# Kernel tuning notes

Hardware: AMD Instinct MI355X
Metric: run time of the kernel (lower is better)

The kernel has to match this reference:

```python
import jax, jax.numpy as jnp
import numpy as np

NF, NG, NH, NR, HS = 6, 32, 16, 15, 256
NT, NS = 1000, 2000


def _linear_init(k, fan_in, fan_out):
    s = 1.0 / np.sqrt(fan_in)
    kw, kb = jax.random.split(k)
    W = jax.random.uniform(kw, (fan_in, fan_out), minval=-s, maxval=s, dtype=jnp.float32)
    b = jax.random.uniform(kb, (fan_out,), minval=-s, maxval=s, dtype=jnp.float32)
    return W, b


def setup_inputs() -> dict:
    key = jax.random.key(0)
    ks = jax.random.split(key, 12)
    # forcings: Prcp, Evp, T1(min temp), T2(max temp), Rad, Hum; ensure Prcp>=0 and T2>T1
    base = jax.random.normal(ks[0], (NT, NS)) * 10.0
    spread = jax.random.uniform(ks[1], (NT, NS)) * 5.0 + 0.5
    prcp = jax.random.uniform(ks[2], (NT, NS)) * 10.0
    evp = jax.random.uniform(ks[3], (NT, NS)) * 3.0
    rad = jax.random.uniform(ks[4], (NT, NS))
    hum = jax.random.uniform(ks[5], (NT, NS))
    x = jnp.stack([prcp, evp, base - spread, base + spread, rad, hum], axis=-1).astype(jnp.float32)
    xc = jax.random.normal(ks[6], (NS, NG), dtype=jnp.float32)
    W_fc, b_fc = _linear_init(ks[7], NG, HS)
    W_r, b_r = _linear_init(ks[8], HS, NH * (NR + 1))
    W_g, b_g = _linear_init(ks[9], HS, NH * 9)
    W_kin, b_kin = _linear_init(ks[10], 4, HS)
    W_kout, b_kout = _linear_init(ks[11], HS, NH * 1)
    return dict(x=x, xc=xc, W_fc=W_fc, b_fc=b_fc, W_r=W_r, b_r=b_r,
                W_g=W_g, b_g=b_g, W_kin=W_kin, b_kin=b_kin,
                W_kout=W_kout, b_kout=b_kout)


def reference(x, xc, W_fc, b_fc, W_r, b_r, W_g, b_g, W_kin, b_kin, W_kout, b_kout):
    nt, ns, _ = x.shape
    Prcp, Evp, T1, T2 = x[..., 0], x[..., 1], x[..., 2], x[..., 3]
    f = x[..., 2:]                                   # [nt, ns, 4]

    # --- getParam (eval mode: DropMask is identity) ---
    state = xc @ W_fc + b_fc                         # [ns, hs]
    pK = jnp.tanh(f @ W_kin + b_kin + state) @ W_kout + b_kout   # [nt, ns, nh]
    km = jnp.exp(pK)                                 # melt rate per step
    g = jnp.tanh(state)
    pG = g @ W_g + b_g                               # [ns, 9*nh]
    sl = lambda i: pG[..., i * NH:(i + 1) * NH]
    kp = jax.nn.sigmoid(sl(0))
    ks_ = jax.nn.sigmoid(sl(1))
    kd = jax.nn.sigmoid(sl(2))
    gd = jax.nn.sigmoid(sl(3))
    gl = (jax.nn.sigmoid(sl(4)) * 10.0) ** 3
    qb = jax.nn.relu(sl(5)) / 10.0
    ga = jax.nn.softmax(sl(6), axis=-1)
    gi = jnp.clip(sl(7) / 6.0 + 0.5, 0.0, 1.0) / 2.0   # hardsigmoid/2
    ge = jax.nn.relu(sl(8))

    # one-peak routing weights over nr lags: [nr, ns, nh], sums to 1 over lag
    pR = (g @ W_r + b_r).reshape(ns, NH, NR + 1)
    loc = jax.nn.sigmoid(pR[..., 0]) * NR            # peak location in [0, nr]
    lags = jnp.arange(NR, dtype=x.dtype)
    wR = jax.nn.softmax(pR[..., 1:] - (lags - loc[..., None]) ** 2, axis=-1)
    paramR = jnp.transpose(wR, (2, 0, 1))            # [nr, ns, nh]

    # --- divideP: split precip into snow / liquid by the fraction of [T1,T2] above 0C ---
    vL = jnp.clip(T2 / jnp.maximum(T2 - T1, 1e-6), 0.0, 1.0)
    Pl = (Prcp * vL)[..., None]                      # [nt, ns, 1]
    Ps = (Prcp * (1.0 - vL))[..., None]
    Ev = Evp[..., None]

    # --- bucket.step recurrence over time via scan ---
    def step(carry, inp):
        Sf, Ss, Sd = carry
        ps, pl, ev, kmt = inp
        Sf1 = Sf + ps                                # snow bucket
        qf = jnp.minimum(Sf1, kmt)                   # melt
        Sf2 = Sf1 - qf
        Pin = pl + qf                                # liquid input
        H = jax.nn.relu(Ss + Pin * (1.0 - gi) - ev * ge)   # shallow bucket
        qp = jax.nn.relu(H - gl) * kp                # saturation-excess quick flow
        qo = jnp.minimum(H, gl) * ks_                # shallow drainage
        Ss2 = H - qp - qo
        D = Sd + Pin * gi + qo * gd                  # deep bucket
        qd = D * kd + qb                             # baseflow
        Sd2 = D * (1.0 - kd)
        qTot = qp + qo * (1.0 - gd) + qd             # qp + qs + qd
        return (Sf2, Ss2, Sd2), qTot

    z = jnp.zeros((ns, NH), dtype=x.dtype)
    _, qTot = jax.lax.scan(step, (z, z, z), (Ps, Pl, Ev, km))   # [nt, ns, nh]

    # --- windowed routing convolution + mixture over buckets ---
    # out[j, s] = sum_{i<nr} sum_h qTot[j+i, s, h] * paramR[i, s, h] * ga[s, h]
    W = paramR * ga[None]                            # [nr, ns, nh]
    L = nt - NR + 1
    out = jnp.zeros((L, ns), dtype=x.dtype)
    for i in range(NR):                              # small fixed lag loop
        out = out + jnp.einsum('tsh,sh->ts', qTot[i:i + L], W[i])
    return out
```

## Files before the change

kernel.cpp:

```cpp
#include <hip/hip_runtime.h>
#include <hip/hip_bf16.h>
#include <hip/hip_fp16.h>

#define NG 32
#define NH 16
#define NR 15
#define HS 256
#define NT 1000
#define NS 2000
#define LOUT (NT - NR + 1)
#define TC 40
#define SPB 8
#define NCH (NT / TC)
#define NTP 1001

typedef __attribute__((ext_vector_type(8))) short bhalf8;
typedef __attribute__((ext_vector_type(4))) float f32x4;
typedef __attribute__((ext_vector_type(2))) float f32x2;
typedef __attribute__((ext_vector_type(4))) unsigned short us4;
typedef __attribute__((ext_vector_type(8))) unsigned short us8;

__device__ __forceinline__ float fast_rcp(float x) { return __builtin_amdgcn_rcpf(x); }
__device__ __forceinline__ float fast_tanh(float x) {
    float e = __expf(2.0f * x);
    return 1.0f - 2.0f * fast_rcp(e + 1.0f);
}
__device__ __forceinline__ float fast_sigmoid(float x) {
    return fast_rcp(1.0f + __expf(-x));
}
__device__ __forceinline__ short f2bf(float f) {
    __bf16 h = (__bf16)f;
    return __builtin_bit_cast(short, h);
}
__device__ __forceinline__ float h2f(unsigned short u) {
    return (float)__builtin_bit_cast(_Float16, u);
}
__device__ __forceinline__ unsigned short f2h(float f) {
    return __builtin_bit_cast(unsigned short, (_Float16)f);
}

__global__ __launch_bounds__(256) void k_prep(const float* __restrict__ x,
                                              float* __restrict__ xT) {
    int s0 = blockIdx.x * 16;
    int t0 = blockIdx.y * 64;
    int tid = threadIdx.x;
    __shared__ float sX[64][97];
    for (int g = tid; g < 64 * 24; g += 256) {
        int tl = g / 24, c4 = g - tl * 24;
        if (t0 + tl < NT) {
            float4 v = *(const float4*)(x + ((size_t)(t0 + tl) * NS + s0) * 6 + c4 * 4);
            sX[tl][c4 * 4 + 0] = v.x;
            sX[tl][c4 * 4 + 1] = v.y;
            sX[tl][c4 * 4 + 2] = v.z;
            sX[tl][c4 * 4 + 3] = v.w;
        }
    }
    __syncthreads();
    int tl = tid & 63;
    int t = t0 + tl;
    if (t < NT) {
#pragma unroll
        for (int p = 0; p < 4; ++p) {
            int sl = (tid >> 6) + p * 4;
            const float* r = &sX[tl][sl * 6];
            size_t base = ((size_t)(s0 + sl) * 6) * NT + t;
            xT[base + 0 * NT] = r[0];
            xT[base + 1 * NT] = r[1];
            xT[base + 2 * NT] = r[2];
            xT[base + 3 * NT] = r[3];
            xT[base + 4 * NT] = r[4];
            xT[base + 5 * NT] = r[5];
        }
    }
}

__global__ __launch_bounds__(256) void k_site(
    const float* __restrict__ xc, const float* __restrict__ W_fc, const float* __restrict__ b_fc,
    const float* __restrict__ W_r, const float* __restrict__ b_r,
    const float* __restrict__ W_g, const float* __restrict__ b_g,
    const float* __restrict__ b_kin,
    float* __restrict__ state2, float* __restrict__ params, float* __restrict__ wfir)
{
    int s = blockIdx.x, tid = threadIdx.x;
    __shared__ float sXc[NG];
    __shared__ float sG[HS];
    __shared__ float sPG[144];
    __shared__ float sPR[256];
    if (tid < NG) sXc[tid] = xc[s * NG + tid];
    __syncthreads();
    float st = b_fc[tid];
#pragma unroll
    for (int g = 0; g < NG; ++g) st += sXc[g] * W_fc[g * HS + tid];
    state2[s * HS + tid] = st + b_kin[tid];
    float gv = fast_tanh(st);
    sG[tid] = gv;
    __syncthreads();
    {
        float a = b_r[tid];
#pragma unroll 8
        for (int u = 0; u < HS; ++u) a += sG[u] * W_r[u * 256 + tid];
        sPR[tid] = a;
    }
    if (tid < 144) {
        float a = b_g[tid];
#pragma unroll 8
        for (int u = 0; u < HS; ++u) a += sG[u] * W_g[u * 144 + tid];
        sPG[tid] = a;
    }
    __syncthreads();
    if (tid < NH) {
        int h = tid;
        float m = -1e30f;
        for (int k = 0; k < NH; ++k) m = fmaxf(m, sPG[96 + k]);
        float sum = 0.f;
        for (int k = 0; k < NH; ++k) sum += __expf(sPG[96 + k] - m);
        float ga = __expf(sPG[96 + h] - m) * fast_rcp(sum);
        float kp = fast_sigmoid(sPG[h]);
        float ks = fast_sigmoid(sPG[16 + h]);
        float kd = fast_sigmoid(sPG[32 + h]);
        float gd = fast_sigmoid(sPG[48 + h]);
        float glv = fast_sigmoid(sPG[64 + h]) * 10.0f;
        float gl = glv * glv * glv;
        float qb = fmaxf(sPG[80 + h], 0.f) * 0.1f;
        float gi = fminf(fmaxf(sPG[112 + h] * (1.0f / 6.0f) + 0.5f, 0.f), 1.f) * 0.5f;
        float ge = fmaxf(sPG[128 + h], 0.f);
        float* P = params + s * 128;
        P[0 * 16 + h] = kp;  P[1 * 16 + h] = ks;  P[2 * 16 + h] = kd;  P[3 * 16 + h] = gd;
        P[4 * 16 + h] = gl;  P[5 * 16 + h] = qb;  P[6 * 16 + h] = gi;  P[7 * 16 + h] = ge;
        float loc = fast_sigmoid(sPR[h * 16 + 0]) * 15.0f;
        float l[NR];
        float mm = -1e30f;
#pragma unroll
        for (int i = 0; i < NR; ++i) {
            float d = (float)i - loc;
            l[i] = sPR[h * 16 + 1 + i] - d * d;
            mm = fmaxf(mm, l[i]);
        }
        float ssum = 0.f;
#pragma unroll
        for (int i = 0; i < NR; ++i) { l[i] = __expf(l[i] - mm); ssum += l[i]; }
        float r = fast_rcp(ssum) * ga;
#pragma unroll
        for (int i = 0; i < NR; ++i) wfir[s * (NR * NH) + i * NH + h] = l[i] * r;
    }
}

__global__ __launch_bounds__(256) void k_km(
    const float* __restrict__ xT, const float* __restrict__ state2,
    const float* __restrict__ W_kin, const float* __restrict__ W_kout,
    const float* __restrict__ b_kout, _Float16* __restrict__ kmh)
{
    const float Ck = 2.8853900817779268f;
    int s = blockIdx.x, tid = threadIdx.x;
    int wave = tid >> 6, lane = tid & 63;
    int r15 = lane & 15, kg = lane >> 4;

    f32x2 st[2][4], w0[2][4], w1[2][4], w2[2][4], w3[2][4];
    bhalf8 Bf[2];
    float csp = 0.f;
#pragma unroll
    for (int q = 0; q < 2; ++q) {
        int u0 = (2 * wave + q) * 32 + kg * 8;
#pragma unroll
        for (int e = 0; e < 4; ++e) {
            int u = u0 + 2 * e;
            st[q][e] = *(const f32x2*)(state2 + s * HS + u) * Ck;
            w0[q][e] = *(const f32x2*)(W_kin + 0 * HS + u) * Ck;
            w1[q][e] = *(const f32x2*)(W_kin + 1 * HS + u) * Ck;
            w2[q][e] = *(const f32x2*)(W_kin + 2 * HS + u) * Ck;
            w3[q][e] = *(const f32x2*)(W_kin + 3 * HS + u) * Ck;
            float wa = W_kout[(u)     * NH + r15];
            float wb = W_kout[(u + 1) * NH + r15];
            csp += wa + wb;
            Bf[q][2 * e]     = f2bf(-2.0f * wa);
            Bf[q][2 * e + 1] = f2bf(-2.0f * wb);
        }
    }
    __shared__ float sCS[4][4][16];
    sCS[wave][kg][r15] = csp;
    __syncthreads();
    float bk2 = b_kout[r15];
#pragma unroll
    for (int w = 0; w < 4; ++w)
#pragma unroll
        for (int k = 0; k < 4; ++k) bk2 += sCS[w][k][r15];

    const float* fpl = xT + ((size_t)s * 6 + 2) * NT;
    _Float16* kp = kmh + (size_t)s * NT * NH;

    __shared__ f32x4 sRed[2][4][4][64];

    for (int tg = 0; tg < 16; ++tg) {
        int buf = tg & 1;
#pragma unroll
        for (int tile = 0; tile < 4; ++tile) {
            int t = tg * 64 + tile * 16 + r15;
            int tcl = t < NT ? t : NT - 1;
            float f0 = fpl[tcl];
            float f1 = fpl[NT + tcl];
            float f2 = fpl[2 * NT + tcl];
            float f3 = fpl[3 * NT + tcl];
            f32x4 acc = {0.f, 0.f, 0.f, 0.f};
#pragma unroll
            for (int q = 0; q < 2; ++q) {
                bhalf8 A;
#pragma unroll
                for (int e = 0; e < 4; ++e) {
                    f32x2 p = st[q][e];
                    p += f0 * w0[q][e];
                    p += f1 * w1[q][e];
                    p += f2 * w2[q][e];
                    p += f3 * w3[q][e];
                    f32x2 ex = {__builtin_amdgcn_exp2f(p.x), __builtin_amdgcn_exp2f(p.y)};
                    f32x2 e1 = ex + 1.0f;
                    A[2 * e]     = f2bf(fast_rcp(e1.x));
                    A[2 * e + 1] = f2bf(fast_rcp(e1.y));
                }
                acc = __builtin_amdgcn_mfma_f32_16x16x32_bf16(A, Bf[q], acc, 0, 0, 0);
            }
            sRed[buf][tile][wave][lane] = acc;
        }
        __syncthreads();
        {
            f32x4 a0 = sRed[buf][wave][0][lane];
            f32x4 a1 = sRed[buf][wave][1][lane];
            f32x4 a2 = sRed[buf][wave][2][lane];
            f32x4 a3 = sRed[buf][wave][3][lane];
            f32x4 acc = (a0 + a1) + (a2 + a3);
            int tb = tg * 64 + wave * 16;
#pragma unroll
            for (int j = 0; j < 4; ++j) {
                int tt = tb + kg * 4 + j;
                if (tt < NT) kp[(size_t)tt * NH + r15] = (_Float16)__expf(acc[j] + bk2);
            }
        }
    }
}

__global__ __launch_bounds__(128) void k_scan(
    const float* __restrict__ params, const float* __restrict__ xT,
    _Float16* __restrict__ kmh)
{
    int tid = threadIdx.x;
    int sl = tid >> 4, h = tid & 15;
    int S0 = blockIdx.x * SPB;
    __shared__ __align__(16) unsigned short sKmH[2][TC][128];
    __shared__ __align__(16) float sF[2][3][SPB][TC];

    const float* P = params + (size_t)(S0 + sl) * 128;
    float kp = P[h], ks = P[16 + h], kd = P[32 + h], gd = P[48 + h];
    float gl = P[64 + h], qb = P[80 + h], gi = P[96 + h], ge = P[112 + h];
    float gi1 = 1.f - gi, gd1 = 1.f - gd, kd1 = 1.f - kd;
    float Sf = 0.f, Ss = 0.f, Sd = 0.f;

    us4 vkm[10];
    float4 fP, fE, fT1, fT2;
    int fsite = tid / 10, ftcq = tid - fsite * 10;
    size_t fbase = ((size_t)(S0 + (fsite < SPB ? fsite : 0)) * 6) * NT + ftcq * 4;

    auto LOAD = [&](int t0) {
#pragma unroll
        for (int r = 0; r < 10; ++r) {
            int g = r * 128 + tid;
            int site = g / 160;
            int rem = g - site * 160;
            int tc = rem >> 2, h0 = (rem & 3) << 2;
            vkm[r] = *(const us4*)(kmh + (((size_t)(S0 + site) * NT + t0 + tc) * NH + h0));
        }
        if (tid < 80) {
            fP  = *(const float4*)(xT + fbase + t0);
            fE  = *(const float4*)(xT + fbase + (size_t)NT + t0);
            fT1 = *(const float4*)(xT + fbase + 2 * (size_t)NT + t0);
            fT2 = *(const float4*)(xT + fbase + 3 * (size_t)NT + t0);
        }
    };
    auto STORE_LDS = [&](int b) {
#pragma unroll
        for (int r = 0; r < 10; ++r) {
            int g = r * 128 + tid;
            int site = g / 160;
            int rem = g - site * 160;
            int tc = rem >> 2, h0 = (rem & 3) << 2;
            *(us4*)&sKmH[b][tc][site * 16 + h0] = vkm[r];
        }
        if (tid < 80) {
            float4 ps, pl;
            {
                float den = fmaxf(fT2.x - fT1.x, 1e-6f);
                float vL = fminf(fmaxf(fT2.x * fast_rcp(den), 0.f), 1.f);
                pl.x = fP.x * vL; ps.x = fP.x - pl.x;
            }
            {
                float den = fmaxf(fT2.y - fT1.y, 1e-6f);
                float vL = fminf(fmaxf(fT2.y * fast_rcp(den), 0.f), 1.f);
                pl.y = fP.y * vL; ps.y = fP.y - pl.y;
            }
            {
                float den = fmaxf(fT2.z - fT1.z, 1e-6f);
                float vL = fminf(fmaxf(fT2.z * fast_rcp(den), 0.f), 1.f);
                pl.z = fP.z * vL; ps.z = fP.z - pl.z;
            }
            {
                float den = fmaxf(fT2.w - fT1.w, 1e-6f);
                float vL = fminf(fmaxf(fT2.w * fast_rcp(den), 0.f), 1.f);
                pl.w = fP.w * vL; ps.w = fP.w - pl.w;
            }
            *(float4*)&sF[b][0][fsite][ftcq * 4] = ps;
            *(float4*)&sF[b][1][fsite][ftcq * 4] = pl;
            *(float4*)&sF[b][2][fsite][ftcq * 4] = fE;
        }
    };

    size_t qbase = ((size_t)(S0 + sl) * NT) * NH + h;

    LOAD(0);
    STORE_LDS(0);
    __syncthreads();
    for (int c = 0; c < NCH; ++c) {
        int b = c & 1;
        if (c + 1 < NCH) LOAD((c + 1) * TC);
        int t0 = c * TC;
#pragma unroll 8
        for (int tc = 0; tc < TC; ++tc) {
            float ps = sF[b][0][sl][tc], pl = sF[b][1][sl][tc], ev = sF[b][2][sl][tc];
            float kmv = h2f(sKmH[b][tc][tid]);
            Sf += ps;
            float qf = fminf(Sf, kmv);
            Sf -= qf;
            float Pin = pl + qf;
            float H = fmaxf(Ss + Pin * gi1 - ev * ge, 0.f);
            float qp = fmaxf(H - gl, 0.f) * kp;
            float qo = fminf(H, gl) * ks;
            Ss = H - qp - qo;
            float D = Sd + Pin * gi + qo * gd;
            float qd = D * kd + qb;
            Sd = D * kd1;
            kmh[qbase + (size_t)(t0 + tc) * NH] = (_Float16)(qp + qo * gd1 + qd);
        }
        if (c + 1 < NCH) {
            STORE_LDS((c + 1) & 1);
            __syncthreads();
        }
    }
}

__global__ __launch_bounds__(256) void k_fir(
    const _Float16* __restrict__ kmh, const float* __restrict__ wfir,
    float* __restrict__ outT)
{
    int s = blockIdx.x, tid = threadIdx.x;
    __shared__ float sQ[NH * NTP];
    __shared__ float sW[NR * NH];
    const us8* src = (const us8*)(kmh + (size_t)s * NT * NH);
    for (int g = tid; g < NT * NH / 8; g += 256) {
        us8 v = src[g];
        int t = g >> 1, h0 = (g & 1) << 3;
#pragma unroll
        for (int e = 0; e < 8; ++e)
            sQ[(h0 + e) * NTP + t] = h2f(v[e]);
    }
    if (tid < NR * NH) sW[tid] = wfir[(size_t)s * NR * NH + tid];
    __syncthreads();
#pragma unroll
    for (int c = 0; c < 4; ++c) {
        int tau = tid + 256 * c;
        if (tau < LOUT) {
            float acc = 0.f;
#pragma unroll
            for (int hh = 0; hh < NH; ++hh) {
                const float* q = sQ + hh * NTP + tau;
#pragma unroll
                for (int i = 0; i < NR; ++i) acc += q[i] * sW[i * 16 + hh];
            }
            outT[(size_t)s * LOUT + tau] = acc;
        }
    }
}

__global__ __launch_bounds__(256) void k_tr(const float* __restrict__ outT,
                                            float* __restrict__ out)
{
    int s0 = blockIdx.x * 64, t0 = blockIdx.y * 16, tid = threadIdx.x;
    __shared__ float sT[16][65];
    for (int g = tid; g < 64 * 16; g += 256) {
        int sl = g >> 4, tl = g & 15;
        int s = s0 + sl, t = t0 + tl;
        sT[tl][sl] = (s < NS && t < LOUT) ? outT[(size_t)s * LOUT + t] : 0.f;
    }
    __syncthreads();
    int ss = tid & 63;
#pragma unroll
    for (int p = 0; p < 4; ++p) {
        int tl = (tid >> 6) + p * 4;
        int t = t0 + tl, s = s0 + ss;
        if (t < LOUT && s < NS) out[(size_t)t * NS + s] = sT[tl][ss];
    }
}

extern "C" void kernel_launch(void* const* d_in, const int* in_sizes, int n_in,
                              void* d_out, int out_size, void* d_ws, size_t ws_size,
                              hipStream_t stream) {
    const float* x      = (const float*)d_in[0];
    const float* xc     = (const float*)d_in[1];
    const float* W_fc   = (const float*)d_in[2];
    const float* b_fc   = (const float*)d_in[3];
    const float* W_r    = (const float*)d_in[4];
    const float* b_r    = (const float*)d_in[5];
    const float* W_g    = (const float*)d_in[6];
    const float* b_g    = (const float*)d_in[7];
    const float* W_kin  = (const float*)d_in[8];
    const float* b_kin  = (const float*)d_in[9];
    const float* W_kout = (const float*)d_in[10];
    const float* b_kout = (const float*)d_in[11];
    float* out = (float*)d_out;

    float* ws     = (float*)d_ws;
    float* state2 = ws;
    float* params = state2 + (size_t)NS * HS;
    float* wfir   = params + (size_t)NS * 128;
    float* xT     = wfir + (size_t)NS * NR * NH;
    _Float16* kmh = (_Float16*)(xT + (size_t)NS * 6 * NT);
    float* outT   = (float*)(kmh + (size_t)NS * NT * NH);

    k_prep<<<dim3(NS / 16, (NT + 63) / 64), 256, 0, stream>>>(x, xT);
    k_site<<<NS, 256, 0, stream>>>(xc, W_fc, b_fc, W_r, b_r, W_g, b_g, b_kin,
                                   state2, params, wfir);
    k_km<<<NS, 256, 0, stream>>>(xT, state2, W_kin, W_kout, b_kout, kmh);
    k_scan<<<NS / SPB, 128, 0, stream>>>(params, xT, kmh);
    k_fir<<<NS, 256, 0, stream>>>(kmh, wfir, outT);
    k_tr<<<dim3((NS + 63) / 64, (LOUT + 15) / 16), 256, 0, stream>>>(outT, out);
}
```

Before: 327.4 us.

## Register-block FIR over four outputs per thread with fp16 LDS storage

The routing FIR kernel now keeps the qTot history in LDS as raw fp16 in padded rows, which halves LDS footprint and allows vectorized 4-wide loads. Each thread computes four consecutive outputs, loading a 20-element window per bucket into registers and reusing it across lags. This cuts the redundant LDS reads of the old one-output-per-thread loop. It costs more registers and adds padding zero-fill and per-element half-to-float conversions in the inner loop.

```diff
diff --git a/kernel.cpp b/kernel.cpp
--- a/kernel.cpp
+++ b/kernel.cpp
@@ -12,7 +12,7 @@
 #define TC 40
 #define SPB 8
 #define NCH (NT / TC)
-#define NTP 1001
+#define QROW 1048
 
 typedef __attribute__((ext_vector_type(8))) short bhalf8;
 typedef __attribute__((ext_vector_type(4))) float f32x4;
@@ -349,32 +349,48 @@
     float* __restrict__ outT)
 {
     int s = blockIdx.x, tid = threadIdx.x;
-    __shared__ float sQ[NH * NTP];
+    __shared__ unsigned short sQ[NH][QROW];
     __shared__ float sW[NR * NH];
+    for (int idx = tid; idx < NH * (QROW - NT); idx += 256) {
+        int h = idx / (QROW - NT), j = idx - h * (QROW - NT);
+        sQ[h][NT + j] = 0;
+    }
     const us8* src = (const us8*)(kmh + (size_t)s * NT * NH);
     for (int g = tid; g < NT * NH / 8; g += 256) {
         us8 v = src[g];
         int t = g >> 1, h0 = (g & 1) << 3;
 #pragma unroll
-        for (int e = 0; e < 8; ++e)
-            sQ[(h0 + e) * NTP + t] = h2f(v[e]);
+        for (int e = 0; e < 8; ++e) sQ[h0 + e][t] = v[e];
     }
     if (tid < NR * NH) sW[tid] = wfir[(size_t)s * NR * NH + tid];
     __syncthreads();
-#pragma unroll
-    for (int c = 0; c < 4; ++c) {
-        int tau = tid + 256 * c;
-        if (tau < LOUT) {
-            float acc = 0.f;
-#pragma unroll
-            for (int hh = 0; hh < NH; ++hh) {
-                const float* q = sQ + hh * NTP + tau;
-#pragma unroll
-                for (int i = 0; i < NR; ++i) acc += q[i] * sW[i * 16 + hh];
-            }
-            outT[(size_t)s * LOUT + tau] = acc;
-        }
-    }
+
+    int tau0 = tid * 4;
+    float a0 = 0.f, a1 = 0.f, a2 = 0.f, a3 = 0.f;
+#pragma unroll
+    for (int h = 0; h < NH; ++h) {
+        float q[20];
+#pragma unroll
+        for (int r = 0; r < 5; ++r) {
+            us4 v = *(const us4*)&sQ[h][tau0 + 4 * r];
+            q[4 * r + 0] = h2f(v[0]);
+            q[4 * r + 1] = h2f(v[1]);
+            q[4 * r + 2] = h2f(v[2]);
+            q[4 * r + 3] = h2f(v[3]);
+        }
+#pragma unroll
+        for (int i = 0; i < NR; ++i) {
+            float w = sW[i * 16 + h];
+            a0 += q[i] * w;
+            a1 += q[i + 1] * w;
+            a2 += q[i + 2] * w;
+            a3 += q[i + 3] * w;
+        }
+    }
+    if (tau0 + 0 < LOUT) outT[(size_t)s * LOUT + tau0 + 0] = a0;
+    if (tau0 + 1 < LOUT) outT[(size_t)s * LOUT + tau0 + 1] = a1;
+    if (tau0 + 2 < LOUT) outT[(size_t)s * LOUT + tau0 + 2] = a2;
+    if (tau0 + 3 < LOUT) outT[(size_t)s * LOUT + tau0 + 3] = a3;
 }
 
 __global__ __launch_bounds__(256) void k_tr(const float* __restrict__ outT,
```

Measured after the change: 1.246 ms. +280.5%, slower.
